# Optimization experiments

Measured on AMD Instinct MI355X. Metric: run time of the kernel, lower is better.

## Reference

```python
import jax, jax.numpy as jnp
import numpy as np

B, S, E, H, D = 384, 128, 512, 4, 128  # batch, seq(block), embed, heads, head_dim


def setup_inputs() -> dict:
    key = jax.random.key(0)
    ks = jax.random.split(key, 6)
    scale = 1.0 / np.sqrt(E)  # lecun_normal-ish fan-in scaling
    return {
        "x": jax.random.normal(ks[0], (B, S, E), dtype=jnp.float32),
        "Wq": jax.random.normal(ks[1], (E, E), dtype=jnp.float32) * scale,
        "bq": jnp.zeros((E,), dtype=jnp.float32),
        "Wk": jax.random.normal(ks[2], (E, E), dtype=jnp.float32) * scale,
        "bk": jnp.zeros((E,), dtype=jnp.float32),
        "Wv": jax.random.normal(ks[3], (E, E), dtype=jnp.float32) * scale,
        "bv": jnp.zeros((E,), dtype=jnp.float32),
        "Wo": jax.random.normal(ks[4], (E, E), dtype=jnp.float32) * scale,
        "bo": jnp.zeros((E,), dtype=jnp.float32),
    }


def reference(x, Wq, bq, Wk, bk, Wv, bv, Wo, bo):
    # Projections, then split heads: [B,S,E] -> [B,S,H,D]
    q = (x @ Wq + bq).reshape(B, S, H, D)
    k = (x @ Wk + bk).reshape(B, S, H, D)
    v = (x @ Wv + bv).reshape(B, S, H, D)
    # NOTE: original applies no 1/sqrt(D) scaling and no mask.
    scores = jnp.einsum("BSHD,BTHD->BHST", q, k)  # [B,H,S,T]
    weights = jax.nn.softmax(scores, axis=-1)
    out = jnp.einsum("BHST,BTHD->BSHD", weights, v).reshape(B, S, E)
    return out @ Wo + bo
```

## Files before the change

kernel.cpp:

```cpp
#include <hip/hip_runtime.h>
#include <hip/hip_bf16.h>
#include <cstdint>


#define EMB 512

typedef __attribute__((ext_vector_type(4))) float    f32x4;
typedef __attribute__((ext_vector_type(8))) _Float16 f16x8;

#define MFMA16(a, b, c) __builtin_amdgcn_mfma_f32_16x16x32_f16((a), (b), (c), 0, 0, 0)

__device__ __forceinline__ int swz128(int row, int col) {
    return row * 128 + (col ^ (((row >> 2) & 3) << 4));
}
__device__ __forceinline__ int swz64(int row, int col) {
    return row * 64 + (col ^ (((row >> 2) & 3) << 4));
}

__device__ __forceinline__ void gld_lds16(const _Float16* g, _Float16* l) {
    __builtin_amdgcn_global_load_lds(
        (const __attribute__((address_space(1))) void*)g,
        (__attribute__((address_space(3))) void*)l, 16, 0, 0);
}

__device__ __forceinline__ void stage64(_Float16* lds, const _Float16* gbase,
                                        int grow0, int k0, int wave, int lane) {
#pragma unroll
    for (int i = 0; i < 4; ++i) {
        int idx = wave * 256 + i * 64 + lane;
        int n   = idx >> 3;
        int kb  = (idx & 7) ^ (((n >> 2) & 3) << 1);
        gld_lds16(gbase + (grow0 + n) * EMB + k0 + kb * 8,
                  lds + wave * 2048 + i * 512);
    }
}

__device__ __forceinline__ void stage128(_Float16* lds, const _Float16* gbase,
                                         long grow0, int gstride, int gcol0,
                                         int wave, int lane) {
#pragma unroll
    for (int i = 0; i < 8; ++i) {
        int idx = wave * 512 + i * 64 + lane;
        int n   = idx >> 4;
        int kb  = (idx & 15) ^ (((n >> 2) & 3) << 1);
        gld_lds16(gbase + (grow0 + n) * gstride + gcol0 + kb * 8,
                  lds + wave * 4096 + i * 512);
    }
}

#define ZACC(A)                                   \
    _Pragma("unroll") for (int _i = 0; _i < 2; ++_i) \
    _Pragma("unroll") for (int _j = 0; _j < 8; ++_j) \
        A[_i][_j] = (f32x4){0.f, 0.f, 0.f, 0.f};

__global__ void k_cvt_x(const float* __restrict__ x, _Float16* __restrict__ xh) {
    long i = ((long)blockIdx.x * 256 + threadIdx.x) * 8;
    f32x4 a = *(const f32x4*)(x + i);
    f32x4 b = *(const f32x4*)(x + i + 4);
    f16x8 o;
    o[0] = (_Float16)a[0]; o[1] = (_Float16)a[1];
    o[2] = (_Float16)a[2]; o[3] = (_Float16)a[3];
    o[4] = (_Float16)b[0]; o[5] = (_Float16)b[1];
    o[6] = (_Float16)b[2]; o[7] = (_Float16)b[3];
    *(f16x8*)(xh + i) = o;
}

__global__ void k_transpose_w(const float* __restrict__ W, _Float16* __restrict__ Wt) {
    __shared__ float t[32][33];
    int tid = threadIdx.x;
    int tx = tid & 31, ty = tid >> 5;
    int k0 = blockIdx.x * 32, n0 = blockIdx.y * 32;
#pragma unroll
    for (int i = 0; i < 4; ++i)
        t[ty + i * 8][tx] = W[(k0 + ty + i * 8) * EMB + n0 + tx];
    __syncthreads();
#pragma unroll
    for (int i = 0; i < 4; ++i)
        Wt[(n0 + ty + i * 8) * EMB + k0 + tx] = (_Float16)t[tx][ty + i * 8];
}

__global__ __launch_bounds__(256, 4)
void k_qkv(const _Float16* __restrict__ xh, const _Float16* __restrict__ Wqkvt,
           const float* __restrict__ bq, const float* __restrict__ bk,
           const float* __restrict__ bv,
           _Float16* __restrict__ qb, _Float16* __restrict__ kb,
           _Float16* __restrict__ vtb) {
    __shared__ _Float16 SA[128 * 64];
    __shared__ _Float16 SB[128 * 64];
    const int tid = threadIdx.x, wave = tid >> 6, lane = tid & 63;
    const int l15 = lane & 15, quad = lane >> 4;
    const int bi = blockIdx.x;
    const int bb = bi / 12, j = bi - bb * 12;
    const int m0 = bb * 128;
    const bool vswap = (j >= 8);
    const _Float16* As = vswap ? SB : SA;
    const _Float16* Bs = vswap ? SA : SB;
    f32x4 acc[2][8];
    ZACC(acc);
    for (int k0 = 0; k0 < EMB; k0 += 64) {
        stage64(SA, xh, m0, k0, wave, lane);
        stage64(SB, Wqkvt, j * 128, k0, wave, lane);
        __syncthreads();
#pragma unroll
        for (int ktl = 0; ktl < 2; ++ktl) {
            int cb = ktl * 32 + quad * 8;
            f16x8 a0 = *(const f16x8*)&As[swz64(wave * 32 + l15, cb)];
            f16x8 a1 = *(const f16x8*)&As[swz64(wave * 32 + 16 + l15, cb)];
#pragma unroll
            for (int nt = 0; nt < 8; ++nt) {
                f16x8 bbf = *(const f16x8*)&Bs[swz64(nt * 16 + l15, cb)];
                acc[0][nt] = MFMA16(a0, bbf, acc[0][nt]);
                acc[1][nt] = MFMA16(a1, bbf, acc[1][nt]);
            }
        }
        __syncthreads();
    }
    if (!vswap) {
        const float* bias = (j < 4) ? bq : bk;
        _Float16* dst = (j < 4) ? qb : kb;
        const int nc0 = (j & 3) * 128;
#pragma unroll
        for (int nt = 0; nt < 8; ++nt) {
            int col = nt * 16 + l15;
            float bv_ = bias[nc0 + col];
#pragma unroll
            for (int mt = 0; mt < 2; ++mt)
#pragma unroll
                for (int r = 0; r < 4; ++r) {
                    int row = wave * 32 + mt * 16 + quad * 4 + r;
                    dst[(long)(m0 + row) * EMB + nc0 + col] =
                        (_Float16)(acc[mt][nt][r] + bv_);
                }
        }
    } else {
        const int hv = j - 8;
        _Float16* dst = vtb + (long)(bb * 4 + hv) * 128 * 128;
#pragma unroll
        for (int mt = 0; mt < 2; ++mt)
#pragma unroll
            for (int r = 0; r < 4; ++r) {
                int d = wave * 32 + mt * 16 + quad * 4 + r;
                float bvv = bv[hv * 128 + d];
#pragma unroll
                for (int nt = 0; nt < 8; ++nt) {
                    int t = nt * 16 + l15;
                    dst[d * 128 + t] = (_Float16)(acc[mt][nt][r] + bvv);
                }
            }
    }
}

__global__ __launch_bounds__(256, 2)
void k_core(const _Float16* __restrict__ qb, const _Float16* __restrict__ kb,
            const _Float16* __restrict__ vtb, _Float16* __restrict__ attn) {
    __shared__ _Float16 SK[128 * 128];
    __shared__ _Float16 SV[128 * 128];
    const int tid = threadIdx.x, wave = tid >> 6, lane = tid & 63;
    const int l15 = lane & 15, quad = lane >> 4;
    const int b = blockIdx.x >> 2, h = blockIdx.x & 3;
    const int sRow0 = b * 128, wRow0 = h * 128;
    f32x4 acc[2][8];

    stage128(SK, kb, sRow0, EMB, wRow0, wave, lane);
    stage128(SV, vtb, (long)(b * 4 + h) * 128, 128, 0, wave, lane);
    __syncthreads();

    ZACC(acc);
#pragma unroll
    for (int kt = 0; kt < 4; ++kt) {
        int ca = kt * 32 + quad * 8;
        const _Float16* qrow = qb + (long)(sRow0 + wave * 32 + l15) * EMB + wRow0 + ca;
        f16x8 q0 = *(const f16x8*)qrow;
        f16x8 q1 = *(const f16x8*)(qrow + 16 * EMB);
#pragma unroll
        for (int nt = 0; nt < 8; ++nt) {
            f16x8 kf = *(const f16x8*)&SK[swz128(nt * 16 + l15, ca)];
            acc[0][nt] = MFMA16(q0, kf, acc[0][nt]);
            acc[1][nt] = MFMA16(q1, kf, acc[1][nt]);
        }
    }
#pragma unroll
    for (int mt = 0; mt < 2; ++mt)
#pragma unroll
        for (int r = 0; r < 4; ++r) {
            float mx = acc[mt][0][r];
#pragma unroll
            for (int nt = 1; nt < 8; ++nt) mx = fmaxf(mx, acc[mt][nt][r]);
            mx = fmaxf(mx, __shfl_xor(mx, 1));
            mx = fmaxf(mx, __shfl_xor(mx, 2));
            mx = fmaxf(mx, __shfl_xor(mx, 4));
            mx = fmaxf(mx, __shfl_xor(mx, 8));
            float sm = 0.f;
#pragma unroll
            for (int nt = 0; nt < 8; ++nt) {
                float e = __expf(acc[mt][nt][r] - mx);
                acc[mt][nt][r] = e;
                sm += e;
            }
            sm += __shfl_xor(sm, 1);
            sm += __shfl_xor(sm, 2);
            sm += __shfl_xor(sm, 4);
            sm += __shfl_xor(sm, 8);
            float inv = 1.0f / sm;
#pragma unroll
            for (int nt = 0; nt < 8; ++nt) acc[mt][nt][r] *= inv;
        }
    __syncthreads();

#pragma unroll
    for (int mt = 0; mt < 2; ++mt)
#pragma unroll
        for (int nt = 0; nt < 8; ++nt) {
            int col = nt * 16 + l15;
#pragma unroll
            for (int r = 0; r < 4; ++r) {
                int row = wave * 32 + mt * 16 + quad * 4 + r;
                SK[swz128(row, col)] = (_Float16)acc[mt][nt][r];
            }
        }
    __syncthreads();

    ZACC(acc);
#pragma unroll
    for (int kt = 0; kt < 4; ++kt) {
        int ca = kt * 32 + quad * 8;
        int rp = wave * 32 + l15;
        f16x8 p0 = *(const f16x8*)&SK[swz128(rp, ca)];
        f16x8 p1 = *(const f16x8*)&SK[swz128(rp + 16, ca)];
#pragma unroll
        for (int nt = 0; nt < 8; ++nt) {
            f16x8 vf = *(const f16x8*)&SV[swz128(nt * 16 + l15, ca)];
            acc[0][nt] = MFMA16(p0, vf, acc[0][nt]);
            acc[1][nt] = MFMA16(p1, vf, acc[1][nt]);
        }
    }
    __syncthreads();

#pragma unroll
    for (int mt = 0; mt < 2; ++mt)
#pragma unroll
        for (int nt = 0; nt < 8; ++nt) {
            int col = nt * 16 + l15;
#pragma unroll
            for (int r = 0; r < 4; ++r) {
                int row = wave * 32 + mt * 16 + quad * 4 + r;
                SK[swz128(row, col)] = (_Float16)acc[mt][nt][r];
            }
        }
    __syncthreads();
#pragma unroll
    for (int i = 0; i < 8; ++i) {
        int idx = i * 256 + tid;
        int row = idx >> 4, col = (idx & 15) * 8;
        f16x8 v = *(const f16x8*)&SK[row * 128 + (col ^ (((row >> 2) & 3) << 4))];
        *(f16x8*)(attn + (long)(sRow0 + row) * EMB + wRow0 + col) = v;
    }
}

__global__ __launch_bounds__(256, 4)
void k_out(const _Float16* __restrict__ attn, const _Float16* __restrict__ Wot,
           const float* __restrict__ bo, float* __restrict__ out) {
    __shared__ _Float16 SA[128 * 64];
    __shared__ _Float16 SB[128 * 64];
    const int tid = threadIdx.x, wave = tid >> 6, lane = tid & 63;
    const int l15 = lane & 15, quad = lane >> 4;
    const int m0 = (blockIdx.x >> 2) * 128, n0 = (blockIdx.x & 3) * 128;
    f32x4 acc[2][8];
    ZACC(acc);
    for (int k0 = 0; k0 < EMB; k0 += 64) {
        stage64(SA, attn, m0, k0, wave, lane);
        stage64(SB, Wot, n0, k0, wave, lane);
        __syncthreads();
#pragma unroll
        for (int ktl = 0; ktl < 2; ++ktl) {
            int ra = wave * 32 + l15;
            int cb = ktl * 32 + quad * 8;
            f16x8 a0 = *(const f16x8*)&SA[swz64(ra, cb)];
            f16x8 a1 = *(const f16x8*)&SA[swz64(ra + 16, cb)];
#pragma unroll
            for (int nt = 0; nt < 8; ++nt) {
                f16x8 bb = *(const f16x8*)&SB[swz64(nt * 16 + l15, cb)];
                acc[0][nt] = MFMA16(a0, bb, acc[0][nt]);
                acc[1][nt] = MFMA16(a1, bb, acc[1][nt]);
            }
        }
        __syncthreads();
    }
#pragma unroll
    for (int nt = 0; nt < 8; ++nt) {
        int col = n0 + nt * 16 + l15;
        float bias = bo[col];
#pragma unroll
        for (int mt = 0; mt < 2; ++mt)
#pragma unroll
            for (int r = 0; r < 4; ++r) {
                int row = m0 + wave * 32 + mt * 16 + quad * 4 + r;
                out[(long)row * EMB + col] = acc[mt][nt][r] + bias;
            }
    }
}

extern "C" void kernel_launch(void* const* d_in, const int* in_sizes, int n_in,
                              void* d_out, int out_size, void* d_ws, size_t ws_size,
                              hipStream_t stream) {
    const float* x  = (const float*)d_in[0];
    const float* Wq = (const float*)d_in[1];
    const float* bq = (const float*)d_in[2];
    const float* Wk = (const float*)d_in[3];
    const float* bk = (const float*)d_in[4];
    const float* Wv = (const float*)d_in[5];
    const float* bv = (const float*)d_in[6];
    const float* Wo = (const float*)d_in[7];
    const float* bo = (const float*)d_in[8];
    float* out = (float*)d_out;

    char* w = (char*)d_ws;
    _Float16* xh    = (_Float16*)(w);
    _Float16* attn  = xh;
    _Float16* Wqkvt = (_Float16*)(w + 50331648);
    _Float16* Wot   = (_Float16*)(w + 51904512);
    _Float16* qb    = (_Float16*)(w + 52428800);
    _Float16* kb    = (_Float16*)(w + 102760448);
    _Float16* vtb   = (_Float16*)(w + 153092096);

    k_cvt_x<<<12288, 256, 0, stream>>>(x, xh);
    dim3 tg(16, 16);
    k_transpose_w<<<tg, 256, 0, stream>>>(Wq, Wqkvt);
    k_transpose_w<<<tg, 256, 0, stream>>>(Wk, Wqkvt + 512 * EMB);
    k_transpose_w<<<tg, 256, 0, stream>>>(Wv, Wqkvt + 1024 * EMB);
    k_transpose_w<<<tg, 256, 0, stream>>>(Wo, Wot);
    k_qkv<<<4608, 256, 0, stream>>>(xh, Wqkvt, bq, bk, bv, qb, kb, vtb);
    k_core<<<1536, 256, 0, stream>>>(qb, kb, vtb, attn);
    k_out<<<1536, 256, 0, stream>>>(attn, Wot, bo, out);
}
```

Measured before the change: 385.3 us.

## Fuse prep kernels, XCD-aware block mapping, LDS-staged stores, drop core LDS staging

Merges the x-conversion and four weight-transpose launches into one prep kernel to cut launch overhead. Remaps block indices in qkv, core and out so that blocks sharing a batch row land on the same XCD, which is meant to improve L2 locality. The qkv epilogue now writes through swizzled LDS for coalesced 16-byte global stores. The core kernel drops the K and V LDS staging in favour of direct global loads, halving its LDS use and raising launch bounds to 4 blocks per CU. This trades LDS reuse for more occupancy and relies on L2/L1 hits for the K and V fragments.

```diff
diff --git a/kernel.cpp b/kernel.cpp
--- a/kernel.cpp
+++ b/kernel.cpp
@@ -35,41 +35,35 @@
     }
 }
 
-__device__ __forceinline__ void stage128(_Float16* lds, const _Float16* gbase,
-                                         long grow0, int gstride, int gcol0,
-                                         int wave, int lane) {
-#pragma unroll
-    for (int i = 0; i < 8; ++i) {
-        int idx = wave * 512 + i * 64 + lane;
-        int n   = idx >> 4;
-        int kb  = (idx & 15) ^ (((n >> 2) & 3) << 1);
-        gld_lds16(gbase + (grow0 + n) * gstride + gcol0 + kb * 8,
-                  lds + wave * 4096 + i * 512);
-    }
-}
-
 #define ZACC(A)                                   \
     _Pragma("unroll") for (int _i = 0; _i < 2; ++_i) \
     _Pragma("unroll") for (int _j = 0; _j < 8; ++_j) \
         A[_i][_j] = (f32x4){0.f, 0.f, 0.f, 0.f};
 
-__global__ void k_cvt_x(const float* __restrict__ x, _Float16* __restrict__ xh) {
-    long i = ((long)blockIdx.x * 256 + threadIdx.x) * 8;
-    f32x4 a = *(const f32x4*)(x + i);
-    f32x4 b = *(const f32x4*)(x + i + 4);
-    f16x8 o;
-    o[0] = (_Float16)a[0]; o[1] = (_Float16)a[1];
-    o[2] = (_Float16)a[2]; o[3] = (_Float16)a[3];
-    o[4] = (_Float16)b[0]; o[5] = (_Float16)b[1];
-    o[6] = (_Float16)b[2]; o[7] = (_Float16)b[3];
-    *(f16x8*)(xh + i) = o;
-}
-
-__global__ void k_transpose_w(const float* __restrict__ W, _Float16* __restrict__ Wt) {
+__global__ void k_prep(const float* __restrict__ x, _Float16* __restrict__ xh,
+                       const float* __restrict__ Wq, const float* __restrict__ Wk,
+                       const float* __restrict__ Wv, const float* __restrict__ Wo,
+                       _Float16* __restrict__ Wqkvt, _Float16* __restrict__ Wot) {
     __shared__ float t[32][33];
-    int tid = threadIdx.x;
-    int tx = tid & 31, ty = tid >> 5;
-    int k0 = blockIdx.x * 32, n0 = blockIdx.y * 32;
+    const int g = blockIdx.x, tid = threadIdx.x;
+    if (g < 12288) {
+        long i = ((long)g * 256 + tid) * 8;
+        f32x4 a = *(const f32x4*)(x + i);
+        f32x4 b = *(const f32x4*)(x + i + 4);
+        f16x8 o;
+        o[0] = (_Float16)a[0]; o[1] = (_Float16)a[1];
+        o[2] = (_Float16)a[2]; o[3] = (_Float16)a[3];
+        o[4] = (_Float16)b[0]; o[5] = (_Float16)b[1];
+        o[6] = (_Float16)b[2]; o[7] = (_Float16)b[3];
+        *(f16x8*)(xh + i) = o;
+        return;
+    }
+    const int tb = g - 12288;
+    const int z = tb >> 8, t2 = tb & 255;
+    const float* W = (z == 0) ? Wq : (z == 1) ? Wk : (z == 2) ? Wv : Wo;
+    _Float16* Wt = (z < 3) ? (Wqkvt + (long)z * 512 * EMB) : Wot;
+    const int tx = tid & 31, ty = tid >> 5;
+    const int k0 = (t2 & 15) * 32, n0 = (t2 >> 4) * 32;
 #pragma unroll
     for (int i = 0; i < 4; ++i)
         t[ty + i * 8][tx] = W[(k0 + ty + i * 8) * EMB + n0 + tx];
@@ -85,12 +79,14 @@
            const float* __restrict__ bv,
            _Float16* __restrict__ qb, _Float16* __restrict__ kb,
            _Float16* __restrict__ vtb) {
-    __shared__ _Float16 SA[128 * 64];
-    __shared__ _Float16 SB[128 * 64];
+    __shared__ _Float16 S[2][128 * 64];
+    _Float16* SA = S[0];
+    _Float16* SB = S[1];
     const int tid = threadIdx.x, wave = tid >> 6, lane = tid & 63;
     const int l15 = lane & 15, quad = lane >> 4;
-    const int bi = blockIdx.x;
-    const int bb = bi / 12, j = bi - bb * 12;
+    const int g = blockIdx.x;
+    const int xcd = g & 7, r = g >> 3;
+    const int bb = xcd * 48 + r / 12, j = r % 12;
     const int m0 = bb * 128;
     const bool vswap = (j >= 8);
     const _Float16* As = vswap ? SB : SA;
@@ -115,55 +111,69 @@
         }
         __syncthreads();
     }
+    _Float16* SC = &S[0][0];
     if (!vswap) {
         const float* bias = (j < 4) ? bq : bk;
+        const int nc0 = (j & 3) * 128;
+#pragma unroll
+        for (int nt = 0; nt < 8; ++nt) {
+            int col = nt * 16 + l15;
+            float bz = bias[nc0 + col];
+#pragma unroll
+            for (int mt = 0; mt < 2; ++mt)
+#pragma unroll
+                for (int rr = 0; rr < 4; ++rr) {
+                    int row = wave * 32 + mt * 16 + quad * 4 + rr;
+                    SC[swz128(row, col)] = (_Float16)(acc[mt][nt][rr] + bz);
+                }
+        }
+        __syncthreads();
         _Float16* dst = (j < 4) ? qb : kb;
-        const int nc0 = (j & 3) * 128;
-#pragma unroll
-        for (int nt = 0; nt < 8; ++nt) {
-            int col = nt * 16 + l15;
-            float bv_ = bias[nc0 + col];
-#pragma unroll
-            for (int mt = 0; mt < 2; ++mt)
-#pragma unroll
-                for (int r = 0; r < 4; ++r) {
-                    int row = wave * 32 + mt * 16 + quad * 4 + r;
-                    dst[(long)(m0 + row) * EMB + nc0 + col] =
-                        (_Float16)(acc[mt][nt][r] + bv_);
-                }
+#pragma unroll
+        for (int i = 0; i < 8; ++i) {
+            int idx = i * 256 + tid;
+            int row = idx >> 4, col = (idx & 15) * 8;
+            f16x8 v = *(const f16x8*)&SC[row * 128 + (col ^ (((row >> 2) & 3) << 4))];
+            *(f16x8*)(dst + (long)(m0 + row) * EMB + nc0 + col) = v;
         }
     } else {
         const int hv = j - 8;
+#pragma unroll
+        for (int mt = 0; mt < 2; ++mt)
+#pragma unroll
+            for (int rr = 0; rr < 4; ++rr) {
+                int row = wave * 32 + mt * 16 + quad * 4 + rr;
+                float bz = bv[hv * 128 + row];
+#pragma unroll
+                for (int nt = 0; nt < 8; ++nt) {
+                    int col = nt * 16 + l15;
+                    SC[swz128(row, col)] = (_Float16)(acc[mt][nt][rr] + bz);
+                }
+            }
+        __syncthreads();
         _Float16* dst = vtb + (long)(bb * 4 + hv) * 128 * 128;
 #pragma unroll
-        for (int mt = 0; mt < 2; ++mt)
-#pragma unroll
-            for (int r = 0; r < 4; ++r) {
-                int d = wave * 32 + mt * 16 + quad * 4 + r;
-                float bvv = bv[hv * 128 + d];
-#pragma unroll
-                for (int nt = 0; nt < 8; ++nt) {
-                    int t = nt * 16 + l15;
-                    dst[d * 128 + t] = (_Float16)(acc[mt][nt][r] + bvv);
-                }
-            }
-    }
-}
-
-__global__ __launch_bounds__(256, 2)
+        for (int i = 0; i < 8; ++i) {
+            int idx = i * 256 + tid;
+            int row = idx >> 4, col = (idx & 15) * 8;
+            f16x8 v = *(const f16x8*)&SC[row * 128 + (col ^ (((row >> 2) & 3) << 4))];
+            *(f16x8*)(dst + row * 128 + col) = v;
+        }
+    }
+}
+
+__global__ __launch_bounds__(256, 4)
 void k_core(const _Float16* __restrict__ qb, const _Float16* __restrict__ kb,
             const _Float16* __restrict__ vtb, _Float16* __restrict__ attn) {
-    __shared__ _Float16 SK[128 * 128];
-    __shared__ _Float16 SV[128 * 128];
+    __shared__ _Float16 SP[128 * 128];
     const int tid = threadIdx.x, wave = tid >> 6, lane = tid & 63;
     const int l15 = lane & 15, quad = lane >> 4;
-    const int b = blockIdx.x >> 2, h = blockIdx.x & 3;
+    const int g = blockIdx.x;
+    const int xcd = g & 7, r = g >> 3;
+    const int b = xcd * 48 + (r >> 2), h = r & 3;
     const int sRow0 = b * 128, wRow0 = h * 128;
+    const _Float16* vt = vtb + (long)(b * 4 + h) * 128 * 128;
     f32x4 acc[2][8];
-
-    stage128(SK, kb, sRow0, EMB, wRow0, wave, lane);
-    stage128(SV, vtb, (long)(b * 4 + h) * 128, 128, 0, wave, lane);
-    __syncthreads();
 
     ZACC(acc);
 #pragma unroll
@@ -174,7 +184,7 @@
         f16x8 q1 = *(const f16x8*)(qrow + 16 * EMB);
 #pragma unroll
         for (int nt = 0; nt < 8; ++nt) {
-            f16x8 kf = *(const f16x8*)&SK[swz128(nt * 16 + l15, ca)];
+            f16x8 kf = *(const f16x8*)(kb + (long)(sRow0 + nt * 16 + l15) * EMB + wRow0 + ca);
             acc[0][nt] = MFMA16(q0, kf, acc[0][nt]);
             acc[1][nt] = MFMA16(q1, kf, acc[1][nt]);
         }
@@ -182,10 +192,10 @@
 #pragma unroll
     for (int mt = 0; mt < 2; ++mt)
 #pragma unroll
-        for (int r = 0; r < 4; ++r) {
-            float mx = acc[mt][0][r];
-#pragma unroll
-            for (int nt = 1; nt < 8; ++nt) mx = fmaxf(mx, acc[mt][nt][r]);
+        for (int rr = 0; rr < 4; ++rr) {
+            float mx = acc[mt][0][rr];
+#pragma unroll
+            for (int nt = 1; nt < 8; ++nt) mx = fmaxf(mx, acc[mt][nt][rr]);
             mx = fmaxf(mx, __shfl_xor(mx, 1));
             mx = fmaxf(mx, __shfl_xor(mx, 2));
             mx = fmaxf(mx, __shfl_xor(mx, 4));
@@ -193,8 +203,8 @@
             float sm = 0.f;
 #pragma unroll
             for (int nt = 0; nt < 8; ++nt) {
-                float e = __expf(acc[mt][nt][r] - mx);
-                acc[mt][nt][r] = e;
+                float e = __expf(acc[mt][nt][rr] - mx);
+                acc[mt][nt][rr] = e;
                 sm += e;
             }
             sm += __shfl_xor(sm, 1);
@@ -203,9 +213,8 @@
             sm += __shfl_xor(sm, 8);
             float inv = 1.0f / sm;
 #pragma unroll
-            for (int nt = 0; nt < 8; ++nt) acc[mt][nt][r] *= inv;
-        }
-    __syncthreads();
+            for (int nt = 0; nt < 8; ++nt) acc[mt][nt][rr] *= inv;
+        }
 
 #pragma unroll
     for (int mt = 0; mt < 2; ++mt)
@@ -213,9 +222,9 @@
         for (int nt = 0; nt < 8; ++nt) {
             int col = nt * 16 + l15;
 #pragma unroll
-            for (int r = 0; r < 4; ++r) {
-                int row = wave * 32 + mt * 16 + quad * 4 + r;
-                SK[swz128(row, col)] = (_Float16)acc[mt][nt][r];
+            for (int rr = 0; rr < 4; ++rr) {
+                int row = wave * 32 + mt * 16 + quad * 4 + rr;
+                SP[swz128(row, col)] = (_Float16)acc[mt][nt][rr];
             }
         }
     __syncthreads();
@@ -225,11 +234,11 @@
     for (int kt = 0; kt < 4; ++kt) {
         int ca = kt * 32 + quad * 8;
         int rp = wave * 32 + l15;
-        f16x8 p0 = *(const f16x8*)&SK[swz128(rp, ca)];
-        f16x8 p1 = *(const f16x8*)&SK[swz128(rp + 16, ca)];
-#pragma unroll
-        for (int nt = 0; nt < 8; ++nt) {
-            f16x8 vf = *(const f16x8*)&SV[swz128(nt * 16 + l15, ca)];
+        f16x8 p0 = *(const f16x8*)&SP[swz128(rp, ca)];
+        f16x8 p1 = *(const f16x8*)&SP[swz128(rp + 16, ca)];
+#pragma unroll
+        for (int nt = 0; nt < 8; ++nt) {
+            f16x8 vf = *(const f16x8*)(vt + (nt * 16 + l15) * 128 + ca);
             acc[0][nt] = MFMA16(p0, vf, acc[0][nt]);
             acc[1][nt] = MFMA16(p1, vf, acc[1][nt]);
         }
@@ -242,9 +251,9 @@
         for (int nt = 0; nt < 8; ++nt) {
             int col = nt * 16 + l15;
 #pragma unroll
-            for (int r = 0; r < 4; ++r) {
-                int row = wave * 32 + mt * 16 + quad * 4 + r;
-                SK[swz128(row, col)] = (_Float16)acc[mt][nt][r];
+            for (int rr = 0; rr < 4; ++rr) {
+                int row = wave * 32 + mt * 16 + quad * 4 + rr;
+                SP[swz128(row, col)] = (_Float16)acc[mt][nt][rr];
             }
         }
     __syncthreads();
@@ -252,7 +261,7 @@
     for (int i = 0; i < 8; ++i) {
         int idx = i * 256 + tid;
         int row = idx >> 4, col = (idx & 15) * 8;
-        f16x8 v = *(const f16x8*)&SK[row * 128 + (col ^ (((row >> 2) & 3) << 4))];
+        f16x8 v = *(const f16x8*)&SP[row * 128 + (col ^ (((row >> 2) & 3) << 4))];
         *(f16x8*)(attn + (long)(sRow0 + row) * EMB + wRow0 + col) = v;
     }
 }
@@ -264,7 +273,9 @@
     __shared__ _Float16 SB[128 * 64];
     const int tid = threadIdx.x, wave = tid >> 6, lane = tid & 63;
     const int l15 = lane & 15, quad = lane >> 4;
-    const int m0 = (blockIdx.x >> 2) * 128, n0 = (blockIdx.x & 3) * 128;
+    const int g = blockIdx.x;
+    const int xcd = g & 7, r = g >> 3;
+    const int m0 = (xcd * 48 + (r >> 2)) * 128, n0 = (r & 3) * 128;
     f32x4 acc[2][8];
     ZACC(acc);
     for (int k0 = 0; k0 < EMB; k0 += 64) {
@@ -293,9 +304,9 @@
 #pragma unroll
         for (int mt = 0; mt < 2; ++mt)
 #pragma unroll
-            for (int r = 0; r < 4; ++r) {
-                int row = m0 + wave * 32 + mt * 16 + quad * 4 + r;
-                out[(long)row * EMB + col] = acc[mt][nt][r] + bias;
+            for (int rr = 0; rr < 4; ++rr) {
+                int row = m0 + wave * 32 + mt * 16 + quad * 4 + rr;
+                out[(long)row * EMB + col] = acc[mt][nt][rr] + bias;
             }
     }
 }
@@ -323,12 +334,7 @@
     _Float16* kb    = (_Float16*)(w + 102760448);
     _Float16* vtb   = (_Float16*)(w + 153092096);
 
-    k_cvt_x<<<12288, 256, 0, stream>>>(x, xh);
-    dim3 tg(16, 16);
-    k_transpose_w<<<tg, 256, 0, stream>>>(Wq, Wqkvt);
-    k_transpose_w<<<tg, 256, 0, stream>>>(Wk, Wqkvt + 512 * EMB);
-    k_transpose_w<<<tg, 256, 0, stream>>>(Wv, Wqkvt + 1024 * EMB);
-    k_transpose_w<<<tg, 256, 0, stream>>>(Wo, Wot);
+    k_prep<<<13312, 256, 0, stream>>>(x, xh, Wq, Wk, Wv, Wo, Wqkvt, Wot);
     k_qkv<<<4608, 256, 0, stream>>>(xh, Wqkvt, bq, bk, bv, qb, kb, vtb);
     k_core<<<1536, 256, 0, stream>>>(qb, kb, vtb, attn);
     k_out<<<1536, 256, 0, stream>>>(attn, Wot, bo, out);
```

After: 378.7 us. No clear change (-1.7%).
